# Optimization experiments

Hardware: AMD Instinct MI355X
Metric: run time of the kernel (lower is better)

Reference implementation:

```python
import jax, jax.numpy as jnp
import numpy as np


def setup_inputs() -> dict:
    key = jax.random.key(0)
    k1, k2, k3 = jax.random.split(key, 3)
    B, S, D, N = 2, 2048, 1024, 16
    H = D // N  # head_dim = 64
    x = jax.random.normal(k1, (B, S, D), dtype=jnp.float32)
    W_qkv = jax.random.normal(k2, (N, D, 3 * H), dtype=jnp.float32) / np.sqrt(D).astype(np.float32)
    W_out = jax.random.normal(k3, (N, H, D), dtype=jnp.float32) / np.sqrt(D).astype(np.float32)
    return {"x": x, "W_qkv": W_qkv, "W_out": W_out}


def reference(x, W_qkv, W_out):
    B, S, D = x.shape
    head_dim = W_qkv.shape[-1] // 3
    # QKV projection per head: [B, N, S, 3*H]
    qkv = jnp.einsum('bsd,ndh->bnsh', x, W_qkv)
    q, k, v = jnp.split(qkv, 3, axis=-1)  # each [B, N, S, H]
    scale = jnp.asarray(1.0 / np.sqrt(head_dim), dtype=x.dtype)
    attn = jnp.einsum('bnqh,bnkh->bnqk', q, k) * scale  # [B, N, S, S]
    # causal mask: -1e10 above the diagonal (matches buffer in original)
    mask = jnp.asarray(-1e10, dtype=x.dtype) * (1.0 - jnp.tril(jnp.ones((S, S), dtype=x.dtype)))
    attn = jax.nn.softmax(attn + mask, axis=-1)
    out = jnp.einsum('bnqk,bnkh->bnqh', attn, v)  # [B, N, S, H]
    # faithful to original: raw row-major reshape [B,N,S,H] -> [B, N*H, S]
    out = out.reshape(B, -1, S)
    # faithful to original einsum: d kept, n and h summed over W_out
    return jnp.einsum('bds,nhd->bsd', out, W_out)
```

## Files before the change

### kernel.cpp

```cpp
#include <hip/hip_runtime.h>
#include <hip/hip_bf16.h>

#define B_ 2
#define S_ 2048
#define D_ 1024
#define N_ 16
#define H_ 64

typedef unsigned short u16;
typedef unsigned int u32;
typedef __bf16 bf16x8 __attribute__((ext_vector_type(8)));
typedef u16 u16x8 __attribute__((ext_vector_type(8)));
typedef u32 u32x2 __attribute__((ext_vector_type(2)));
typedef u32 u32x4 __attribute__((ext_vector_type(4)));
typedef float f4v __attribute__((ext_vector_type(4)));

__device__ __forceinline__ u16 f2b(float f) {
    u32 u = __builtin_bit_cast(u32, f);
    u32 r = (u + 0x7FFFu + ((u >> 16) & 1u)) >> 16;
    return (u16)r;
}
__device__ __forceinline__ bf16x8 asbf(u16x8 v) { return __builtin_bit_cast(bf16x8, v); }
__device__ __forceinline__ u32 cvtpk(float a, float b) {
    u32 r;
    asm("v_cvt_pk_bf16_f32 %0, %1, %2" : "=v"(r) : "v"(a), "v"(b));
    return r;
}
__device__ __forceinline__ void gload16(const u16* g, u16* l) {
    __builtin_amdgcn_global_load_lds((const __attribute__((address_space(1))) void*)g,
                                     (__attribute__((address_space(3))) void*)l, 16, 0, 0);
}

__global__ __launch_bounds__(256) void k_setup(const float* __restrict__ x,
                                               const float* __restrict__ w,
                                               const float* __restrict__ Wout,
                                               u16* __restrict__ xb,
                                               u16* __restrict__ wt,
                                               float* __restrict__ wsum) {
    __shared__ float T[64][65];
    const int bid = blockIdx.x;
    const int t = threadIdx.x;
    if (bid < 2048) {
        size_t i = ((size_t)bid * 256 + t) * 8;
        float4 f0 = *(const float4*)(x + i);
        float4 f1 = *(const float4*)(x + i + 4);
        u16x8 o;
        o[0] = f2b(f0.x); o[1] = f2b(f0.y); o[2] = f2b(f0.z); o[3] = f2b(f0.w);
        o[4] = f2b(f1.x); o[5] = f2b(f1.y); o[6] = f2b(f1.z); o[7] = f2b(f1.w);
        *(u16x8*)(xb + i) = o;
    } else if (bid < 2816) {
        const int v = bid - 2048;
        const int n = v / 48, rem = v % 48;
        const int jt = rem >> 4, d0 = (rem & 15) * 64;
        const int j0 = jt * 64;
        const float sc = (jt == 0) ? 0.125f * 1.44269504089f : 1.0f;
#pragma unroll
        for (int rep = 0; rep < 4; ++rep) {
            int vv = t + rep * 256;
            int row = vv >> 4, c4 = vv & 15;
            float4 f = *(const float4*)(w + ((size_t)(n * 1024 + d0 + row)) * 192 + j0 + c4 * 4);
            T[row][c4 * 4 + 0] = f.x * sc;
            T[row][c4 * 4 + 1] = f.y * sc;
            T[row][c4 * 4 + 2] = f.z * sc;
            T[row][c4 * 4 + 3] = f.w * sc;
        }
        __syncthreads();
#pragma unroll
        for (int rep = 0; rep < 2; ++rep) {
            int c = t + rep * 256;
            int j = c >> 3, db = c & 7;
            u16x8 o;
#pragma unroll
            for (int e = 0; e < 8; ++e) o[e] = f2b(T[db * 8 + e][j]);
            *(u16x8*)(wt + ((size_t)(n * 192 + j0 + j)) * 1024 + d0 + db * 8) = o;
        }
    } else {
        const int bx = bid - 2816;
        const int dd = t & 15, rr = t >> 4;
        const int d = bx * 16 + dd;
        float s = 0.f;
        for (int r = rr * 64; r < rr * 64 + 64; ++r) s += Wout[(size_t)r * 1024 + d];
        float* red = &T[0][0];
        red[rr * 17 + dd] = s;
        __syncthreads();
        if (rr == 0) {
            float tt = 0.f;
#pragma unroll
            for (int k = 0; k < 16; ++k) tt += red[k * 17 + dd];
            wsum[d] = tt;
        }
    }
}

__global__ __launch_bounds__(512) void k_qkv(const u16* __restrict__ xb,
                                             const u16* __restrict__ wt,
                                             u16* __restrict__ qbuf,
                                             u16* __restrict__ kbuf,
                                             u16* __restrict__ vt) {
    __shared__ u16 As[128 * 64];
    __shared__ u16 Bst[192 * 64];
    const int st = blockIdx.x, n = blockIdx.y;
    const int t = threadIdx.x;
    const int w = t >> 6, lane = t & 63, hi2 = lane >> 4, lo4 = lane & 15;
    const int wm = w >> 2, wn = w & 3;

    const int l8 = lane >> 3, l7 = (lane & 7) * 8;
    const u16* AgL = xb + (size_t)(st * 128 + w * 16 + l8) * 1024 + l7;
    u16* AdL = As + w * 16 * 64;
    const u16* BgL = wt + (size_t)(n * 192 + w * 24 + l8) * 1024 + l7;
    u16* BdL = Bst + w * 24 * 64;

    f4v acc[4][3];
#pragma unroll
    for (int i = 0; i < 4; ++i)
#pragma unroll
        for (int j = 0; j < 3; ++j) acc[i][j] = (f4v){0.f, 0.f, 0.f, 0.f};

    for (int kk = 0; kk < 16; ++kk) {
        __syncthreads();
        const int ko = kk * 64;
        gload16(AgL + ko, AdL);
        gload16(AgL + ko + (size_t)8 * 1024, AdL + 8 * 64);
        gload16(BgL + ko, BdL);
        gload16(BgL + ko + (size_t)8 * 1024, BdL + 8 * 64);
        gload16(BgL + ko + (size_t)16 * 1024, BdL + 16 * 64);
        __syncthreads();
        bf16x8 fa[4][2];
#pragma unroll
        for (int ms = 0; ms < 4; ++ms) {
            const u16* ar = As + (wm * 64 + ms * 16 + lo4) * 64;
            fa[ms][0] = asbf(*(const u16x8*)(ar + hi2 * 8));
            fa[ms][1] = asbf(*(const u16x8*)(ar + hi2 * 8 + 32));
        }
        __builtin_amdgcn_s_setprio(1);
#pragma unroll
        for (int fj = 0; fj < 3; ++fj) {
            const u16* br = Bst + (wn * 48 + fj * 16 + lo4) * 64;
            bf16x8 fb0 = asbf(*(const u16x8*)(br + hi2 * 8));
            bf16x8 fb1 = asbf(*(const u16x8*)(br + hi2 * 8 + 32));
#pragma unroll
            for (int ms = 0; ms < 4; ++ms) {
                acc[ms][fj] = __builtin_amdgcn_mfma_f32_16x16x32_bf16(fa[ms][0], fb0, acc[ms][fj], 0, 0, 0);
                acc[ms][fj] = __builtin_amdgcn_mfma_f32_16x16x32_bf16(fa[ms][1], fb1, acc[ms][fj], 0, 0, 0);
            }
        }
        __builtin_amdgcn_s_setprio(0);
    }

    const int b = st >> 4, s128 = (st & 15) * 128;
    u16* Cs = As;
#pragma unroll
    for (int sec = 0; sec < 3; ++sec) {
        __syncthreads();
#pragma unroll
        for (int fj = 0; fj < 3; ++fj) {
            const int base = wn * 48 + fj * 16;
            if ((base >> 6) == sec) {
                const int col = base - sec * 64 + lo4;
#pragma unroll
                for (int ms = 0; ms < 4; ++ms)
#pragma unroll
                    for (int r = 0; r < 4; ++r)
                        Cs[(wm * 64 + ms * 16 + hi2 * 4 + r) * 64 + col] = f2b(acc[ms][fj][r]);
            }
        }
        __syncthreads();
        if (sec == 2) {
            const int h = t & 63, sb = t >> 6;
            u16x8 o0, o1;
#pragma unroll
            for (int e = 0; e < 8; ++e) o0[e] = Cs[(sb * 16 + e) * 64 + h];
#pragma unroll
            for (int e = 0; e < 8; ++e) o1[e] = Cs[(sb * 16 + 8 + e) * 64 + h];
            u16* dst = vt + ((size_t)(b * 16 + n) * 64 + h) * 2048 + s128 + sb * 16;
            *(u16x8*)dst = o0;
            *(u16x8*)(dst + 8) = o1;
        } else {
            const int row = t >> 2, off = (t & 3) * 16;
            u16* dst = (sec == 0) ? qbuf : kbuf;
            dst += ((size_t)(b * 16 + n) * 2048 + s128 + row) * 64 + off;
            *(u16x8*)dst = *(const u16x8*)(Cs + row * 64 + off);
            *(u16x8*)(dst + 8) = *(const u16x8*)(Cs + row * 64 + off + 8);
        }
    }
}

__global__ __launch_bounds__(256, 4) void k_attn(const u16* __restrict__ qbuf,
                                                 const u16* __restrict__ kbuf,
                                                 const u16* __restrict__ vt,
                                                 const float* __restrict__ wsum,
                                                 float* __restrict__ out) {
    __shared__ u16 SMEM[16384];
    u16* Ks = SMEM;
    u16* Vs = SMEM + 8192;
    const int u = blockIdx.x;
    const int bn = u & 31;
    const int qt = 31 - (int)(u >> 5);
    const int t = threadIdx.x;
    const int w = t >> 6, lane = t & 63, hi2 = lane >> 4, lo4 = lane & 15;
    const int rsw = (lo4 & 7) << 3;

    const int q = qt * 64 + w * 16 + lo4;
    const u16* Qp = qbuf + ((size_t)bn * 2048 + q) * 64;
    bf16x8 bq0 = asbf(*(const u16x8*)(Qp + hi2 * 8));
    bf16x8 bq1 = asbf(*(const u16x8*)(Qp + 32 + hi2 * 8));

    const int srow = t >> 2, q4 = t & 3;
    const int ssw = (srow & 7) << 3;
    const u16* Kg = kbuf + (size_t)bn * 131072 + (size_t)srow * 64 + q4 * 16;
    const u16* Vg = vt + (size_t)bn * 131072 + (size_t)srow * 2048 + q4 * 16;
    const int ko0 = srow * 64 + ((q4 * 16) ^ ssw);
    const int ko1 = srow * 64 + ((q4 * 16 + 8) ^ ssw);
    const int soA = q4 * 2, soB = q4 * 2 + 1;
    const int vsbA = 32 * (soA >> 2) + 16 * (soA & 1) + 4 * ((soA >> 1) & 1);
    const int vsbB = 32 * (soB >> 2) + 16 * (soB & 1) + 4 * ((soB >> 1) & 1);
    const int voA0 = srow * 64 + ((vsbA + 0) ^ ssw);
    const int voA1 = srow * 64 + ((vsbA + 8) ^ ssw);
    const int voB0 = srow * 64 + ((vsbB + 0) ^ ssw);
    const int voB1 = srow * 64 + ((vsbB + 8) ^ ssw);

    f4v accO[4];
#pragma unroll
    for (int i = 0; i < 4; ++i) accO[i] = (f4v){0.f, 0.f, 0.f, 0.f};
    float l = 0.f;
    const int nkb = qt + 1;
    const int npair = (nkb + 1) >> 1;

    u16x8 krA0 = *(const u16x8*)(Kg);
    u16x8 krA1 = *(const u16x8*)(Kg + 8);
    u16x8 krB0 = *(const u16x8*)(Kg + 4096);
    u16x8 krB1 = *(const u16x8*)(Kg + 4096 + 8);
    u16x8 vrA0 = *(const u16x8*)(Vg);
    u16x8 vrA1 = *(const u16x8*)(Vg + 8);
    u16x8 vrB0 = *(const u16x8*)(Vg + 64);
    u16x8 vrB1 = *(const u16x8*)(Vg + 64 + 8);

    for (int pair = 0; pair < npair; ++pair) {
        __syncthreads();
        *(u16x8*)(Ks + ko0) = krA0;
        *(u16x8*)(Ks + ko1) = krA1;
        *(u16x8*)(Ks + 4096 + ko0) = krB0;
        *(u16x8*)(Ks + 4096 + ko1) = krB1;
        {
            u32x4 a0 = __builtin_bit_cast(u32x4, vrA0);
            u32x4 a1 = __builtin_bit_cast(u32x4, vrA1);
            u32x4 b0 = __builtin_bit_cast(u32x4, vrB0);
            u32x4 b1 = __builtin_bit_cast(u32x4, vrB1);
            *(u32x2*)(Vs + voA0) = (u32x2){a0[0], a0[1]};
            *(u32x2*)(Vs + voA1) = (u32x2){a0[2], a0[3]};
            *(u32x2*)(Vs + voB0) = (u32x2){a1[0], a1[1]};
            *(u32x2*)(Vs + voB1) = (u32x2){a1[2], a1[3]};
            *(u32x2*)(Vs + 4096 + voA0) = (u32x2){b0[0], b0[1]};
            *(u32x2*)(Vs + 4096 + voA1) = (u32x2){b0[2], b0[3]};
            *(u32x2*)(Vs + 4096 + voB0) = (u32x2){b1[0], b1[1]};
            *(u32x2*)(Vs + 4096 + voB1) = (u32x2){b1[2], b1[3]};
        }
        if (pair + 1 < npair) {
            const size_t ko = (size_t)(pair + 1) * 8192;
            const int vo = (pair + 1) * 128;
            krA0 = *(const u16x8*)(Kg + ko);
            krA1 = *(const u16x8*)(Kg + ko + 8);
            krB0 = *(const u16x8*)(Kg + ko + 4096);
            krB1 = *(const u16x8*)(Kg + ko + 4096 + 8);
            vrA0 = *(const u16x8*)(Vg + vo);
            vrA1 = *(const u16x8*)(Vg + vo + 8);
            vrB0 = *(const u16x8*)(Vg + vo + 64);
            vrB1 = *(const u16x8*)(Vg + vo + 64 + 8);
        }
        __syncthreads();

#pragma unroll
        for (int sub = 0; sub < 2; ++sub) {
            const int kb = 2 * pair + sub;
            if (kb < nkb) {
                const u16* Kc = Ks + sub * 4096;
                const u16* Vc = Vs + sub * 4096;

                f4v s4[4];
#pragma unroll
                for (int i = 0; i < 4; ++i) s4[i] = (f4v){0.f, 0.f, 0.f, 0.f};
                __builtin_amdgcn_s_setprio(1);
#pragma unroll
                for (int fi = 0; fi < 4; ++fi) {
                    const u16* kr = Kc + (fi * 16 + lo4) * 64;
                    bf16x8 ka0 = asbf(*(const u16x8*)(kr + ((hi2 * 8) ^ rsw)));
                    bf16x8 ka1 = asbf(*(const u16x8*)(kr + ((hi2 * 8 + 32) ^ rsw)));
                    s4[fi] = __builtin_amdgcn_mfma_f32_16x16x32_bf16(ka0, bq0, s4[fi], 0, 0, 0);
                    s4[fi] = __builtin_amdgcn_mfma_f32_16x16x32_bf16(ka1, bq1, s4[fi], 0, 0, 0);
                }
                __builtin_amdgcn_s_setprio(0);

                if (kb == qt) {
#pragma unroll
                    for (int fi = 0; fi < 4; ++fi)
#pragma unroll
                        for (int r = 0; r < 4; ++r) {
                            int kvg = kb * 64 + fi * 16 + hi2 * 4 + r;
                            if (kvg > q) s4[fi][r] = -3.0e38f;
                        }
                }

#pragma unroll
                for (int fi = 0; fi < 4; ++fi)
#pragma unroll
                    for (int r = 0; r < 4; ++r) {
                        float pv = __builtin_exp2f(s4[fi][r]);
                        s4[fi][r] = pv;
                        l += pv;
                    }

                u32x4 p0 = {cvtpk(s4[0][0], s4[0][1]), cvtpk(s4[0][2], s4[0][3]),
                            cvtpk(s4[1][0], s4[1][1]), cvtpk(s4[1][2], s4[1][3])};
                u32x4 p1 = {cvtpk(s4[2][0], s4[2][1]), cvtpk(s4[2][2], s4[2][3]),
                            cvtpk(s4[3][0], s4[3][1]), cvtpk(s4[3][2], s4[3][3])};
                bf16x8 pb0 = __builtin_bit_cast(bf16x8, p0);
                bf16x8 pb1 = __builtin_bit_cast(bf16x8, p1);

                __builtin_amdgcn_s_setprio(1);
#pragma unroll
                for (int fh = 0; fh < 4; ++fh) {
                    const u16* vrw = Vc + (fh * 16 + lo4) * 64;
                    bf16x8 va0 = asbf(*(const u16x8*)(vrw + ((hi2 * 8) ^ rsw)));
                    bf16x8 va1 = asbf(*(const u16x8*)(vrw + ((32 + hi2 * 8) ^ rsw)));
                    accO[fh] = __builtin_amdgcn_mfma_f32_16x16x32_bf16(va0, pb0, accO[fh], 0, 0, 0);
                    accO[fh] = __builtin_amdgcn_mfma_f32_16x16x32_bf16(va1, pb1, accO[fh], 0, 0, 0);
                }
                __builtin_amdgcn_s_setprio(0);
            }
        }
    }

    l += __shfl_xor(l, 16);
    l += __shfl_xor(l, 32);

    __syncthreads();
    float* Osh = (float*)SMEM;
    {
        float inv = 1.f / l;
        const int orl = w * 16 + lo4;
        const int osw = (lo4 & 7) << 2;
        float* Or = Osh + orl * 64;
#pragma unroll
        for (int fh = 0; fh < 4; ++fh) {
            f4v o;
#pragma unroll
            for (int r = 0; r < 4; ++r) o[r] = accO[fh][r] * inv;
            *(f4v*)(Or + ((fh * 16 + hi2 * 4) ^ osw)) = o;
        }
    }
    __syncthreads();
    {
        const int b = bn >> 4, n = bn & 15;
        const int d0 = n * 64 + qt * 2;
        const float wx = wsum[d0], wy = wsum[d0 + 1];
#pragma unroll
        for (int rep = 0; rep < 8; ++rep) {
            int p = rep * 256 + t;
            int h = p & 63, tt = p >> 6;
            const int key = (tt & 7) << 2;
            const int hc = h ^ key;
            float2 o = make_float2(Osh[tt * 64 + hc] * wx,
                                   Osh[(32 + tt) * 64 + hc] * wy);
            *(float2*)(out + ((size_t)b * 2048 + p) * 1024 + d0) = o;
        }
    }
}

extern "C" void kernel_launch(void* const* d_in, const int* in_sizes, int n_in,
                              void* d_out, int out_size, void* d_ws, size_t ws_size,
                              hipStream_t stream) {
    const float* x = (const float*)d_in[0];
    const float* Wqkv = (const float*)d_in[1];
    const float* Wout = (const float*)d_in[2];
    float* out = (float*)d_out;

    char* p = (char*)d_ws;
    float* wsum = (float*)p; p += 4096;
    u16* xb = (u16*)p; p += (size_t)4096 * 1024 * 2;
    u16* wt = (u16*)p; p += (size_t)16 * 192 * 1024 * 2;
    u16* qb_ = (u16*)p; p += (size_t)32 * 2048 * 64 * 2;
    u16* kb_ = (u16*)p; p += (size_t)32 * 2048 * 64 * 2;
    u16* vt_ = (u16*)p; p += (size_t)32 * 2048 * 64 * 2;

    k_setup<<<2880, 256, 0, stream>>>(x, Wqkv, Wout, xb, wt, wsum);
    k_qkv<<<dim3(32, 16), 512, 0, stream>>>(xb, wt, qb_, kb_, vt_);
    k_attn<<<1024, 256, 0, stream>>>(qb_, kb_, vt_, wsum, out);
}
```

Measured before the change: 91.55 us.

## Load K fragments directly from global into registers, bypassing LDS

```diff
diff --git a/kernel.cpp b/kernel.cpp
--- a/kernel.cpp
+++ b/kernel.cpp
@@ -190,9 +190,8 @@
                                                  const u16* __restrict__ vt,
                                                  const float* __restrict__ wsum,
                                                  float* __restrict__ out) {
-    __shared__ u16 SMEM[16384];
-    u16* Ks = SMEM;
-    u16* Vs = SMEM + 8192;
+    __shared__ u16 SMEM[8192];
+    u16* Vs = SMEM;
     const int u = blockIdx.x;
     const int bn = u & 31;
     const int qt = 31 - (int)(u >> 5);
@@ -205,12 +204,11 @@
     bf16x8 bq0 = asbf(*(const u16x8*)(Qp + hi2 * 8));
     bf16x8 bq1 = asbf(*(const u16x8*)(Qp + 32 + hi2 * 8));
 
+    const u16* Kf = kbuf + (size_t)bn * 131072 + (size_t)lo4 * 64 + hi2 * 8;
+
     const int srow = t >> 2, q4 = t & 3;
     const int ssw = (srow & 7) << 3;
-    const u16* Kg = kbuf + (size_t)bn * 131072 + (size_t)srow * 64 + q4 * 16;
     const u16* Vg = vt + (size_t)bn * 131072 + (size_t)srow * 2048 + q4 * 16;
-    const int ko0 = srow * 64 + ((q4 * 16) ^ ssw);
-    const int ko1 = srow * 64 + ((q4 * 16 + 8) ^ ssw);
     const int soA = q4 * 2, soB = q4 * 2 + 1;
     const int vsbA = 32 * (soA >> 2) + 16 * (soA & 1) + 4 * ((soA >> 1) & 1);
     const int vsbB = 32 * (soB >> 2) + 16 * (soB & 1) + 4 * ((soB >> 1) & 1);
@@ -226,10 +224,12 @@
     const int nkb = qt + 1;
     const int npair = (nkb + 1) >> 1;
 
-    u16x8 krA0 = *(const u16x8*)(Kg);
-    u16x8 krA1 = *(const u16x8*)(Kg + 8);
-    u16x8 krB0 = *(const u16x8*)(Kg + 4096);
-    u16x8 krB1 = *(const u16x8*)(Kg + 4096 + 8);
+    u16x8 kf[8];
+#pragma unroll
+    for (int fi = 0; fi < 4; ++fi) {
+        kf[2 * fi] = *(const u16x8*)(Kf + fi * 1024);
+        kf[2 * fi + 1] = *(const u16x8*)(Kf + fi * 1024 + 32);
+    }
     u16x8 vrA0 = *(const u16x8*)(Vg);
     u16x8 vrA1 = *(const u16x8*)(Vg + 8);
     u16x8 vrB0 = *(const u16x8*)(Vg + 64);
@@ -237,10 +237,6 @@
 
     for (int pair = 0; pair < npair; ++pair) {
         __syncthreads();
-        *(u16x8*)(Ks + ko0) = krA0;
-        *(u16x8*)(Ks + ko1) = krA1;
-        *(u16x8*)(Ks + 4096 + ko0) = krB0;
-        *(u16x8*)(Ks + 4096 + ko1) = krB1;
         {
             u32x4 a0 = __builtin_bit_cast(u32x4, vrA0);
             u32x4 a1 = __builtin_bit_cast(u32x4, vrA1);
@@ -256,12 +252,7 @@
             *(u32x2*)(Vs + 4096 + voB1) = (u32x2){b1[2], b1[3]};
         }
         if (pair + 1 < npair) {
-            const size_t ko = (size_t)(pair + 1) * 8192;
             const int vo = (pair + 1) * 128;
-            krA0 = *(const u16x8*)(Kg + ko);
-            krA1 = *(const u16x8*)(Kg + ko + 8);
-            krB0 = *(const u16x8*)(Kg + ko + 4096);
-            krB1 = *(const u16x8*)(Kg + ko + 4096 + 8);
             vrA0 = *(const u16x8*)(Vg + vo);
             vrA1 = *(const u16x8*)(Vg + vo + 8);
             vrB0 = *(const u16x8*)(Vg + vo + 64);
@@ -273,7 +264,6 @@
         for (int sub = 0; sub < 2; ++sub) {
             const int kb = 2 * pair + sub;
             if (kb < nkb) {
-                const u16* Kc = Ks + sub * 4096;
                 const u16* Vc = Vs + sub * 4096;
 
                 f4v s4[4];
@@ -282,13 +272,19 @@
                 __builtin_amdgcn_s_setprio(1);
 #pragma unroll
                 for (int fi = 0; fi < 4; ++fi) {
-                    const u16* kr = Kc + (fi * 16 + lo4) * 64;
-                    bf16x8 ka0 = asbf(*(const u16x8*)(kr + ((hi2 * 8) ^ rsw)));
-                    bf16x8 ka1 = asbf(*(const u16x8*)(kr + ((hi2 * 8 + 32) ^ rsw)));
-                    s4[fi] = __builtin_amdgcn_mfma_f32_16x16x32_bf16(ka0, bq0, s4[fi], 0, 0, 0);
-                    s4[fi] = __builtin_amdgcn_mfma_f32_16x16x32_bf16(ka1, bq1, s4[fi], 0, 0, 0);
+                    s4[fi] = __builtin_amdgcn_mfma_f32_16x16x32_bf16(asbf(kf[2 * fi]), bq0, s4[fi], 0, 0, 0);
+                    s4[fi] = __builtin_amdgcn_mfma_f32_16x16x32_bf16(asbf(kf[2 * fi + 1]), bq1, s4[fi], 0, 0, 0);
                 }
                 __builtin_amdgcn_s_setprio(0);
+
+                if (kb + 1 < nkb) {
+                    const u16* Kt = Kf + (size_t)(kb + 1) * 4096;
+#pragma unroll
+                    for (int fi = 0; fi < 4; ++fi) {
+                        kf[2 * fi] = *(const u16x8*)(Kt + fi * 1024);
+                        kf[2 * fi + 1] = *(const u16x8*)(Kt + fi * 1024 + 32);
+                    }
+                }
 
                 if (kb == qt) {
 #pragma unroll
```

New measurement: 136.4 us. +48.9%, slower.
